# Optimization experiments

Hardware: AMD Instinct MI355X
Metric: run time of the kernel (lower is better)

The kernel has to match this reference:

```python
import jax, jax.numpy as jnp
import numpy as np

B, L, C, R, DK = 8, 2048, 512, 64, 64
H = 2 * C  # hdnSize
NEG = -32767.0  # -2**15 + 1
EPS = 1e-5


def _p(key, shape, std=0.02):
    return (jax.random.normal(key, shape, dtype=jnp.float32) * std)


def setup_inputs() -> dict:
    key = jax.random.key(0)
    ks = jax.random.split(key, 16)
    inp = {
        "x": jax.random.normal(ks[0], (B, L, C), dtype=jnp.float32),
        "maskPAD": jax.random.randint(ks[1], (B, 1, L), 0, 2, dtype=jnp.int32),
        "preScores": jax.random.normal(ks[2], (B, R, R), dtype=jnp.float32),
        "Wp": _p(ks[3], (C, R)), "bp": jnp.zeros((R,), jnp.float32),
        "Wq": _p(ks[4], (C, DK)), "bq": jnp.zeros((DK,), jnp.float32),
        "Wk": _p(ks[5], (C, DK)), "bk": jnp.zeros((DK,), jnp.float32),
        "Wv": _p(ks[6], (C, H)), "bv": jnp.zeros((H,), jnp.float32),
        "Wu": _p(ks[7], (C, H)), "bu": jnp.zeros((H,), jnp.float32),
        "Wo": _p(ks[8], (H, C)), "bo": jnp.zeros((C,), jnp.float32),
        "gamma": jnp.ones((C,), jnp.float32),
        "beta": jnp.zeros((C,), jnp.float32),
    }
    return inp


def reference(x, maskPAD, preScores, Wp, bp, Wq, bq, Wk, bk, Wv, bv, Wu, bu, Wo, bo, gamma, beta):
    # GLU gate: [B,L,H]
    gate = jax.nn.silu(x @ Wu + bu)
    # pseudo-attention logits [B,L,r], masked on padded positions
    pScore = x @ Wp + bp
    pad = (maskPAD[:, 0] == 0)[..., None]  # [B,L,1]
    pScore = jnp.where(pad, NEG, pScore)
    pAlpha = jax.nn.softmax(pScore, axis=1)    # softmax over L (dim=-2)
    pAlpha_ = jax.nn.softmax(pScore, axis=-1)  # softmax over r
    # compress: px [B,r,C]  (== pAlpha.transpose(-1,-2) @ x)
    px = jnp.einsum('blr,blc->brc', pAlpha, x)
    q = jax.nn.silu(px @ Wq + bq)  # [B,r,dk]
    k = jax.nn.silu(px @ Wk + bk)  # [B,r,dk]
    v = jax.nn.silu(px @ Wv + bv)  # [B,r,H]
    scores = jnp.einsum('brd,bsd->brs', q, k) / np.sqrt(DK).astype(np.float32)
    scores = scores + preScores
    alpha = jax.nn.softmax(scores, axis=2)
    z = alpha @ v                                # [B,r,H]
    z = jnp.einsum('blr,brh->blh', pAlpha_, z)   # expand back to [B,L,H]
    z = gate * z
    z = z @ Wo + bo                              # [B,L,C]
    y = x + z
    mu = jnp.mean(y, axis=-1, keepdims=True)
    var = jnp.var(y, axis=-1, keepdims=True)
    out = (y - mu) * jax.lax.rsqrt(var + EPS) * gamma + beta
    return out
```

## Files before the change

kernel.cpp:

```cpp
#include <hip/hip_runtime.h>
#include <hip/hip_bf16.h>

constexpr int B_ = 8;
constexpr int L_ = 2048;
constexpr int C_ = 512;
constexpr int R_ = 64;
constexpr int DK_ = 64;
constexpr int H_ = 1024;
constexpr int M_ = B_ * L_;
constexpr int NQKV_ = 1152;
constexpr float NEG_ = -32767.0f;

__device__ __forceinline__ float toF(float x) { return x; }
__device__ __forceinline__ float toF(__hip_bfloat16 x) { return __bfloat162float(x); }
__device__ __forceinline__ float siluf(float v) { return v / (1.0f + __expf(-v)); }
__device__ __forceinline__ ushort bfbits(float f) {
    __hip_bfloat16 h = __float2bfloat16(f);
    union { __hip_bfloat16 h; ushort u; } cv; cv.h = h; return cv.u;
}
__device__ __forceinline__ float bf2f(ushort u) {
    union { uint u; float f; } cv; cv.u = (uint)u << 16; return cv.f;
}

typedef __attribute__((ext_vector_type(8))) short bf16x8;
typedef __attribute__((ext_vector_type(4))) float f32x4;

#define GLOBAL_AS __attribute__((address_space(1)))
#define LDS_AS    __attribute__((address_space(3)))
__device__ __forceinline__ void glds16(const ushort* g, ushort* l) {
    __builtin_amdgcn_global_load_lds((const GLOBAL_AS void*)g, (LDS_AS void*)l, 16, 0, 0);
}

template <int EPI>
__global__ __launch_bounds__(256) void mfma_gemm5(
    const ushort* __restrict__ A, const ushort* __restrict__ Bt,
    const float* __restrict__ bias,
    const float* __restrict__ residF, const ushort* __restrict__ residB,
    const int* __restrict__ mask,
    ushort* __restrict__ outB, float* __restrict__ outF, float* __restrict__ outF2,
    int Ndim, int Kdim, int gridN, long bBatch)
{
    __shared__ ushort As[2][128 * 32];
    __shared__ ushort Bs[2][128 * 32];

    const int i = blockIdx.x;
    const int G = gridDim.x >> 3;
    const int gi = (gridDim.x & 7) ? i : ((i & 7) * G + (i >> 3));
    const int nt = gi % gridN, mt = gi / gridN;
    const int m0 = mt * 128, n0 = nt * 128;

    const int tid = threadIdx.x;
    const int lane = tid & 63, w = tid >> 6;
    const int wm = (w & 1) * 64, wn = (w >> 1) * 64;
    const int lr = lane & 15, lq = lane >> 4;

    const int sr = lane >> 2;
    const int sc = (lane & 3) * 8;
    const int s0 = w * 2, s1 = w * 2 + 1;

    const ushort* Bp = Bt + (bBatch ? (long)(m0 / L_) * bBatch : 0);
    int br0 = n0 + s0 * 16 + sr; if (br0 >= Ndim) br0 = Ndim - 1;
    int br1 = n0 + s1 * 16 + sr; if (br1 >= Ndim) br1 = Ndim - 1;
    const ushort* a0p = A  + (size_t)(m0 + s0 * 16 + sr) * Kdim + sc;
    const ushort* a1p = A  + (size_t)(m0 + s1 * 16 + sr) * Kdim + sc;
    const ushort* b0p = Bp + (size_t)br0 * Kdim + sc;
    const ushort* b1p = Bp + (size_t)br1 * Kdim + sc;
    const int lo0 = s0 * 512 + lane * 8;
    const int lo1 = s1 * 512 + lane * 8;

    f32x4 acc[4][4];
#pragma unroll
    for (int a = 0; a < 4; ++a)
#pragma unroll
        for (int b = 0; b < 4; ++b) acc[a][b] = (f32x4){0.f, 0.f, 0.f, 0.f};

    glds16(a0p, &As[0][lo0]);
    glds16(a1p, &As[0][lo1]);
    glds16(b0p, &Bs[0][lo0]);
    glds16(b1p, &Bs[0][lo1]);

    int cur = 0;
    for (int k0 = 0; k0 < Kdim; k0 += 32) {
        __syncthreads();
        if (k0 + 32 < Kdim) {
            const int nx = cur ^ 1;
            glds16(a0p + k0 + 32, &As[nx][lo0]);
            glds16(a1p + k0 + 32, &As[nx][lo1]);
            glds16(b0p + k0 + 32, &Bs[nx][lo0]);
            glds16(b1p + k0 + 32, &Bs[nx][lo1]);
        }
        bf16x8 af[4], bf[4];
#pragma unroll
        for (int a = 0; a < 4; ++a)
            af[a] = *(const bf16x8*)&As[cur][(wm + a * 16 + lr) * 32 + lq * 8];
#pragma unroll
        for (int b = 0; b < 4; ++b)
            bf[b] = *(const bf16x8*)&Bs[cur][(wn + b * 16 + lr) * 32 + lq * 8];
#pragma unroll
        for (int a = 0; a < 4; ++a)
#pragma unroll
            for (int b = 0; b < 4; ++b)
                acc[a][b] = __builtin_amdgcn_mfma_f32_16x16x32_bf16(af[a], bf[b], acc[a][b], 0, 0, 0);
        cur ^= 1;
    }

#pragma unroll
    for (int a = 0; a < 4; ++a) {
#pragma unroll
        for (int b = 0; b < 4; ++b) {
            const int col = n0 + wn + b * 16 + lr;
            if (col < Ndim) {
                const float bn = (EPI == 3) ? 0.f : bias[col];
#pragma unroll
                for (int r = 0; r < 4; ++r) {
                    const int row = m0 + wm + a * 16 + lq * 4 + r;
                    float v = acc[a][b][r];
                    if (EPI == 0) {
                        v = siluf(v + bn);
                        outB[(size_t)row * Ndim + col] = bfbits(v);
                    } else if (EPI == 2) {
                        v += bn + residF[(size_t)row * Ndim + col];
                        outB[(size_t)row * Ndim + col] = bfbits(v);
                    } else {
                        v *= bf2f(residB[(size_t)row * Ndim + col]);
                        outB[(size_t)row * Ndim + col] = bfbits(v);
                    }
                }
            }
        }
    }
}

__global__ __launch_bounds__(256) void pscore_gemm(
    const ushort* __restrict__ x16, const ushort* __restrict__ Wpt,
    const float* __restrict__ bp, const int* __restrict__ mask,
    ushort* __restrict__ pAR16, float* __restrict__ pScoreT)
{
    __shared__ ushort As[2][128 * 32];
    __shared__ ushort Bs[2][64 * 32];

    const int i = blockIdx.x;
    const int G = gridDim.x >> 3;
    const int gi = (i & 7) * G + (i >> 3);
    const int m0 = gi * 128;

    const int tid = threadIdx.x;
    const int lane = tid & 63, w = tid >> 6;
    const int lr = lane & 15, lq = lane >> 4;
    const int sr = lane >> 2, sc = (lane & 3) * 8;
    const int s0 = w * 2, s1 = w * 2 + 1;

    const ushort* a0p = x16 + (size_t)(m0 + s0 * 16 + sr) * C_ + sc;
    const ushort* a1p = x16 + (size_t)(m0 + s1 * 16 + sr) * C_ + sc;
    const ushort* bwp = Wpt + (size_t)(w * 16 + sr) * C_ + sc;
    const int lo0 = s0 * 512 + lane * 8;
    const int lo1 = s1 * 512 + lane * 8;
    const int lob = w * 512 + lane * 8;

    f32x4 acc[2][4];
#pragma unroll
    for (int a = 0; a < 2; ++a)
#pragma unroll
        for (int b = 0; b < 4; ++b) acc[a][b] = (f32x4){0.f, 0.f, 0.f, 0.f};

    glds16(a0p, &As[0][lo0]);
    glds16(a1p, &As[0][lo1]);
    glds16(bwp, &Bs[0][lob]);

    int cur = 0;
    for (int k0 = 0; k0 < C_; k0 += 32) {
        __syncthreads();
        if (k0 + 32 < C_) {
            const int nx = cur ^ 1;
            glds16(a0p + k0 + 32, &As[nx][lo0]);
            glds16(a1p + k0 + 32, &As[nx][lo1]);
            glds16(bwp + k0 + 32, &Bs[nx][lob]);
        }
        bf16x8 af[2], bf[4];
#pragma unroll
        for (int a = 0; a < 2; ++a)
            af[a] = *(const bf16x8*)&As[cur][(w * 32 + a * 16 + lr) * 32 + lq * 8];
#pragma unroll
        for (int b = 0; b < 4; ++b)
            bf[b] = *(const bf16x8*)&Bs[cur][(b * 16 + lr) * 32 + lq * 8];
#pragma unroll
        for (int a = 0; a < 2; ++a)
#pragma unroll
            for (int b = 0; b < 4; ++b)
                acc[a][b] = __builtin_amdgcn_mfma_f32_16x16x32_bf16(af[a], bf[b], acc[a][b], 0, 0, 0);
        cur ^= 1;
    }

#pragma unroll
    for (int a = 0; a < 2; ++a) {
#pragma unroll
        for (int r = 0; r < 4; ++r) {
            const int row = m0 + w * 32 + a * 16 + lq * 4 + r;
            const bool dead = (mask[row] == 0);
            const int bb = row >> 11, ll = row & (L_ - 1);
            float v[4];
            float mx = -3.4e38f;
#pragma unroll
            for (int b = 0; b < 4; ++b) {
                const int col = b * 16 + lr;
                float t = acc[a][b][r] + bp[col];
                if (dead) t = NEG_;
                v[b] = t;
                pScoreT[((size_t)bb * R_ + col) * L_ + ll] = t;
                mx = fmaxf(mx, t);
            }
#pragma unroll
            for (int o = 1; o < 16; o <<= 1) mx = fmaxf(mx, __shfl_xor(mx, o, 64));
            float e[4], s = 0.f;
#pragma unroll
            for (int b = 0; b < 4; ++b) { e[b] = __expf(v[b] - mx); s += e[b]; }
#pragma unroll
            for (int o = 1; o < 16; o <<= 1) s += __shfl_xor(s, o, 64);
            const float inv = 1.0f / s;
#pragma unroll
            for (int b = 0; b < 4; ++b)
                pAR16[(size_t)row * R_ + b * 16 + lr] = bfbits(e[b] * inv);
        }
    }
}

__global__ __launch_bounds__(256) void fused_gate_z(
    const ushort* __restrict__ x16, const ushort* __restrict__ Wut,
    const float* __restrict__ bu,
    const ushort* __restrict__ pAR, const ushort* __restrict__ zsT,
    ushort* __restrict__ zg)
{
    __shared__ ushort As[2][128 * 32];
    __shared__ ushort Bs[2][128 * 32];

    const int i = blockIdx.x;
    const int G = gridDim.x >> 3;
    const int gi = (i & 7) * G + (i >> 3);
    constexpr int gridN = H_ / 128;
    const int nt = gi % gridN, mt = gi / gridN;
    const int m0 = mt * 128, n0 = nt * 128;

    const int tid = threadIdx.x;
    const int lane = tid & 63, w = tid >> 6;
    const int wm = (w & 1) * 64, wn = (w >> 1) * 64;
    const int lr = lane & 15, lq = lane >> 4;
    const int sr = lane >> 2, sc = (lane & 3) * 8;
    const int s0 = w * 2, s1 = w * 2 + 1;

    const int bidx = m0 >> 11;
    const ushort* a0p = x16 + (size_t)(m0 + s0 * 16 + sr) * C_ + sc;
    const ushort* a1p = x16 + (size_t)(m0 + s1 * 16 + sr) * C_ + sc;
    const ushort* b0p = Wut + (size_t)(n0 + s0 * 16 + sr) * C_ + sc;
    const ushort* b1p = Wut + (size_t)(n0 + s1 * 16 + sr) * C_ + sc;
    const ushort* zb  = zsT + (size_t)bidx * H_ * R_;
    const ushort* c0p = pAR + (size_t)(m0 + s0 * 16 + sr) * R_ + sc;
    const ushort* c1p = pAR + (size_t)(m0 + s1 * 16 + sr) * R_ + sc;
    const ushort* d0p = zb + (size_t)(n0 + s0 * 16 + sr) * R_ + sc;
    const ushort* d1p = zb + (size_t)(n0 + s1 * 16 + sr) * R_ + sc;
    const int lo0 = s0 * 512 + lane * 8;
    const int lo1 = s1 * 512 + lane * 8;

    f32x4 acc[4][4];
#pragma unroll
    for (int a = 0; a < 4; ++a)
#pragma unroll
        for (int b = 0; b < 4; ++b) acc[a][b] = (f32x4){0.f, 0.f, 0.f, 0.f};

    glds16(c0p, &As[0][lo0]);
    glds16(c1p, &As[0][lo1]);
    glds16(d0p, &Bs[0][lo0]);
    glds16(d1p, &Bs[0][lo1]);

    int cur = 0;
#pragma unroll
    for (int kt = 0; kt < 2; ++kt) {
        __syncthreads();
        if (kt == 0) {
            glds16(c0p + 32, &As[1][lo0]);
            glds16(c1p + 32, &As[1][lo1]);
            glds16(d0p + 32, &Bs[1][lo0]);
            glds16(d1p + 32, &Bs[1][lo1]);
        } else {
            glds16(a0p, &As[0][lo0]);
            glds16(a1p, &As[0][lo1]);
            glds16(b0p, &Bs[0][lo0]);
            glds16(b1p, &Bs[0][lo1]);
        }
        bf16x8 af[4], bf[4];
#pragma unroll
        for (int a = 0; a < 4; ++a)
            af[a] = *(const bf16x8*)&As[cur][(wm + a * 16 + lr) * 32 + lq * 8];
#pragma unroll
        for (int b = 0; b < 4; ++b)
            bf[b] = *(const bf16x8*)&Bs[cur][(wn + b * 16 + lr) * 32 + lq * 8];
#pragma unroll
        for (int a = 0; a < 4; ++a)
#pragma unroll
            for (int b = 0; b < 4; ++b)
                acc[a][b] = __builtin_amdgcn_mfma_f32_16x16x32_bf16(af[a], bf[b], acc[a][b], 0, 0, 0);
        cur ^= 1;
    }

    uint pk[4][4][2];
#pragma unroll
    for (int a = 0; a < 4; ++a)
#pragma unroll
        for (int b = 0; b < 4; ++b) {
            pk[a][b][0] = (uint)bfbits(acc[a][b][0]) | ((uint)bfbits(acc[a][b][1]) << 16);
            pk[a][b][1] = (uint)bfbits(acc[a][b][2]) | ((uint)bfbits(acc[a][b][3]) << 16);
            acc[a][b] = (f32x4){0.f, 0.f, 0.f, 0.f};
        }

    for (int k0 = 0; k0 < C_; k0 += 32) {
        __syncthreads();
        if (k0 + 32 < C_) {
            const int nx = cur ^ 1;
            glds16(a0p + k0 + 32, &As[nx][lo0]);
            glds16(a1p + k0 + 32, &As[nx][lo1]);
            glds16(b0p + k0 + 32, &Bs[nx][lo0]);
            glds16(b1p + k0 + 32, &Bs[nx][lo1]);
        }
        bf16x8 af[4], bf[4];
#pragma unroll
        for (int a = 0; a < 4; ++a)
            af[a] = *(const bf16x8*)&As[cur][(wm + a * 16 + lr) * 32 + lq * 8];
#pragma unroll
        for (int b = 0; b < 4; ++b)
            bf[b] = *(const bf16x8*)&Bs[cur][(wn + b * 16 + lr) * 32 + lq * 8];
#pragma unroll
        for (int a = 0; a < 4; ++a)
#pragma unroll
            for (int b = 0; b < 4; ++b)
                acc[a][b] = __builtin_amdgcn_mfma_f32_16x16x32_bf16(af[a], bf[b], acc[a][b], 0, 0, 0);
        cur ^= 1;
    }

#pragma unroll
    for (int a = 0; a < 4; ++a) {
#pragma unroll
        for (int b = 0; b < 4; ++b) {
            const int col = n0 + wn + b * 16 + lr;
            const float bn = bu[col];
#pragma unroll
            for (int r = 0; r < 4; ++r) {
                const int row = m0 + wm + a * 16 + lq * 4 + r;
                const ushort zu = (ushort)((r & 1) ? (pk[a][b][r >> 1] >> 16)
                                                   : (pk[a][b][r >> 1] & 0xffff));
                const float v = siluf(acc[a][b][r] + bn) * bf2f(zu);
                zg[(size_t)row * H_ + col] = bfbits(v);
            }
        }
    }
}

__global__ __launch_bounds__(256) void x_prep(const float* __restrict__ x,
                                              ushort* __restrict__ x16,
                                              ushort* __restrict__ xT16)
{
    __shared__ float tile[32][33];
    const int tx = threadIdx.x & 31, ty = threadIdx.x >> 5;
    const int c0 = blockIdx.x * 32, l0 = blockIdx.y * 32;
#pragma unroll
    for (int i = 0; i < 32; i += 8) {
        const float v = x[(size_t)(l0 + ty + i) * C_ + c0 + tx];
        tile[ty + i][tx] = v;
        x16[(size_t)(l0 + ty + i) * C_ + c0 + tx] = bfbits(v);
    }
    __syncthreads();
    const int bb = l0 >> 11, ll0 = l0 & (L_ - 1);
#pragma unroll
    for (int i = 0; i < 32; i += 8)
        xT16[((size_t)bb * C_ + c0 + ty + i) * L_ + ll0 + tx] = bfbits(tile[tx][ty + i]);
}

__global__ __launch_bounds__(256) void prep_w(
    const float* __restrict__ Wu, const float* __restrict__ Wo, const float* __restrict__ Wp,
    const float* __restrict__ Wq, const float* __restrict__ bq,
    const float* __restrict__ Wk, const float* __restrict__ bk,
    const float* __restrict__ Wv, const float* __restrict__ bv,
    ushort* __restrict__ Wut, ushort* __restrict__ Wot, ushort* __restrict__ Wpt,
    ushort* __restrict__ Wqkvt, float* __restrict__ bqkv)
{
    int id = blockIdx.x;
    const float* W; ushort* Wt; const float* bsrc = nullptr;
    int K, Nloc, n0, k0, nn0;
    if (id < 512) {
        W = Wu; Wt = Wut; K = 512; Nloc = 1024;
        n0 = (id & 31) * 32; k0 = (id >> 5) * 32; nn0 = n0;
    } else if (id < 1024) {
        id -= 512; W = Wo; Wt = Wot; K = 1024; Nloc = 512;
        n0 = (id & 15) * 32; k0 = (id >> 4) * 32; nn0 = n0;
    } else if (id < 1056) {
        id -= 1024; W = Wp; Wt = Wpt; K = 512; Nloc = 64;
        n0 = (id & 1) * 32; k0 = (id >> 1) * 32; nn0 = n0;
    } else {
        id -= 1056; K = 512; Wt = Wqkvt;
        n0 = (id % 36) * 32; k0 = (id / 36) * 32;
        if (n0 < 64)       { W = Wq; bsrc = bq; Nloc = 64;   nn0 = n0; }
        else if (n0 < 128) { W = Wk; bsrc = bk; Nloc = 64;   nn0 = n0 - 64; }
        else               { W = Wv; bsrc = bv; Nloc = 1024; nn0 = n0 - 128; }
    }
    __shared__ float tile[32][33];
    const int tx = threadIdx.x & 31, ty = threadIdx.x >> 5;
#pragma unroll
    for (int i = 0; i < 32; i += 8)
        tile[ty + i][tx] = W[(size_t)(k0 + ty + i) * Nloc + nn0 + tx];
    __syncthreads();
#pragma unroll
    for (int i = 0; i < 32; i += 8)
        Wt[(size_t)(n0 + ty + i) * K + k0 + tx] = bfbits(tile[tx][ty + i]);
    if (bsrc && k0 == 0 && threadIdx.x < 32) bqkv[n0 + threadIdx.x] = bsrc[nn0 + threadIdx.x];
}

__global__ __launch_bounds__(256) void softmaxL2(const float* __restrict__ pScoreT,
                                                 ushort* __restrict__ pALT)
{
    const size_t br = blockIdx.x;
    const float* row = pScoreT + br * L_;
    ushort* orow = pALT + br * L_;
    const int t = threadIdx.x;
    __shared__ float red[256];

    float v[8];
    float mx = -3.4e38f;
#pragma unroll
    for (int j = 0; j < 8; ++j) { v[j] = row[t + j * 256]; mx = fmaxf(mx, v[j]); }
    red[t] = mx; __syncthreads();
    for (int s = 128; s > 0; s >>= 1) { if (t < s) red[t] = fmaxf(red[t], red[t + s]); __syncthreads(); }
    mx = red[0]; __syncthreads();

    float e[8], sum = 0.f;
#pragma unroll
    for (int j = 0; j < 8; ++j) { e[j] = __expf(v[j] - mx); sum += e[j]; }
    red[t] = sum; __syncthreads();
    for (int s = 128; s > 0; s >>= 1) { if (t < s) red[t] += red[t + s]; __syncthreads(); }
    const float inv = 1.0f / red[0];
#pragma unroll
    for (int j = 0; j < 8; ++j) orow[t + j * 256] = bfbits(e[j] * inv);
}

__global__ __launch_bounds__(512) void compress_mfma(
    const ushort* __restrict__ pALT, const ushort* __restrict__ xT,
    float* __restrict__ parts)
{
    __shared__ ushort As[2][64 * 32];
    __shared__ ushort Bs[2][256 * 32];

    const int bidx = blockIdx.y;
    const int n0 = blockIdx.x * 256;
    const int ks = blockIdx.z;
    const int kbeg = ks * (L_ / 4), kend = kbeg + L_ / 4;
    const int tid = threadIdx.x;
    const int lane = tid & 63, w = tid >> 6;
    const int lr = lane & 15, lq = lane >> 4;
    const int sr = lane >> 2, sc = (lane & 3) * 8;
    const int wm = (w & 1) * 32, wn = (w >> 1) * 64;

    const ushort* Ab = pALT + (size_t)bidx * R_ * L_;
    const ushort* Bb = xT + (size_t)bidx * C_ * L_;

    const int aseg = (w >= 4) ? (w - 4) : 0;
    const ushort* ap = Ab + (size_t)(aseg * 16 + sr) * L_ + sc;
    const int alo = aseg * 512 + lane * 8;
    const ushort* b0p = Bb + (size_t)(n0 + (w * 2) * 16 + sr) * L_ + sc;
    const ushort* b1p = Bb + (size_t)(n0 + (w * 2 + 1) * 16 + sr) * L_ + sc;
    const int blo0 = (w * 2) * 512 + lane * 8;
    const int blo1 = (w * 2 + 1) * 512 + lane * 8;

    f32x4 acc[2][4];
#pragma unroll
    for (int a = 0; a < 2; ++a)
#pragma unroll
        for (int b = 0; b < 4; ++b) acc[a][b] = (f32x4){0.f, 0.f, 0.f, 0.f};

    if (w >= 4) glds16(ap + kbeg, &As[0][alo]);
    glds16(b0p + kbeg, &Bs[0][blo0]);
    glds16(b1p + kbeg, &Bs[0][blo1]);

    int cur = 0;
    for (int k0 = kbeg; k0 < kend; k0 += 32) {
        __syncthreads();
        if (k0 + 32 < kend) {
            const int nx = cur ^ 1;
            if (w >= 4) glds16(ap + k0 + 32, &As[nx][alo]);
            glds16(b0p + k0 + 32, &Bs[nx][blo0]);
            glds16(b1p + k0 + 32, &Bs[nx][blo1]);
        }
        bf16x8 af[2], bf[4];
#pragma unroll
        for (int a = 0; a < 2; ++a)
            af[a] = *(const bf16x8*)&As[cur][(wm + a * 16 + lr) * 32 + lq * 8];
#pragma unroll
        for (int b = 0; b < 4; ++b)
            bf[b] = *(const bf16x8*)&Bs[cur][(wn + b * 16 + lr) * 32 + lq * 8];
#pragma unroll
        for (int a = 0; a < 2; ++a)
#pragma unroll
            for (int b = 0; b < 4; ++b)
                acc[a][b] = __builtin_amdgcn_mfma_f32_16x16x32_bf16(af[a], bf[b], acc[a][b], 0, 0, 0);
        cur ^= 1;
    }
#pragma unroll
    for (int a = 0; a < 2; ++a)
#pragma unroll
        for (int b = 0; b < 4; ++b)
#pragma unroll
            for (int r = 0; r < 4; ++r) {
                const int row = wm + a * 16 + lq * 4 + r;
                const int col = n0 + wn + b * 16 + lr;
                parts[(((size_t)ks * B_ + bidx) * R_ + row) * C_ + col] = acc[a][b][r];
            }
}

__global__ __launch_bounds__(256) void compress_reduce16(const float* __restrict__ parts,
                                                         ushort* __restrict__ px16)
{
    const size_t i = ((size_t)blockIdx.x * 256 + threadIdx.x) * 4;
    constexpr size_t S = (size_t)B_ * R_ * C_;
    const float4 a = *(const float4*)(parts + i);
    const float4 b = *(const float4*)(parts + i + S);
    const float4 c = *(const float4*)(parts + i + 2 * S);
    const float4 d = *(const float4*)(parts + i + 3 * S);
    ushort4 o;
    o.x = bfbits(a.x + b.x + c.x + d.x);
    o.y = bfbits(a.y + b.y + c.y + d.y);
    o.z = bfbits(a.z + b.z + c.z + d.z);
    o.w = bfbits(a.w + b.w + c.w + d.w);
    *(ushort4*)(px16 + i) = o;
}

__global__ __launch_bounds__(256) void attn_fused(
    const ushort* __restrict__ qkv, const float* __restrict__ preS,
    ushort* __restrict__ zsT)
{
    const int b = blockIdx.x >> 6, r = blockIdx.x & 63;
    const int t = threadIdx.x;
    __shared__ float al[R_];
    if (t < 64) {
        const ushort* qr = qkv + (size_t)(b * R_ + r) * NQKV_;
        const ushort* ks = qkv + (size_t)(b * R_ + t) * NQKV_ + 64;
        float acc = 0.f;
#pragma unroll
        for (int d = 0; d < DK_; d += 4) {
            const ushort4 qa = *(const ushort4*)(qr + d);
            const ushort4 ka = *(const ushort4*)(ks + d);
            acc += bf2f(qa.x) * bf2f(ka.x) + bf2f(qa.y) * bf2f(ka.y)
                 + bf2f(qa.z) * bf2f(ka.z) + bf2f(qa.w) * bf2f(ka.w);
        }
        acc = acc * 0.125f + preS[((size_t)b * R_ + r) * R_ + t];
        float mx = acc;
#pragma unroll
        for (int o = 32; o > 0; o >>= 1) mx = fmaxf(mx, __shfl_xor(mx, o, 64));
        float e = __expf(acc - mx);
        float sm = e;
#pragma unroll
        for (int o = 32; o > 0; o >>= 1) sm += __shfl_xor(sm, o, 64);
        al[t] = e / sm;
    }
    __syncthreads();
    float acc[4] = {};
    for (int s = 0; s < R_; ++s) {
        const float a = al[s];
        const ushort* vr = qkv + (size_t)(b * R_ + s) * NQKV_ + 128;
#pragma unroll
        for (int j = 0; j < 4; ++j) acc[j] += a * bf2f(vr[t + j * 256]);
    }
#pragma unroll
    for (int j = 0; j < 4; ++j) {
        const int h = t + j * 256;
        zsT[((size_t)b * H_ + h) * R_ + r] = bfbits(acc[j]);
    }
}

__global__ __launch_bounds__(256) void layernorm(const __hip_bfloat16* __restrict__ y,
                                                 const float* __restrict__ gamma,
                                                 const float* __restrict__ beta,
                                                 float* __restrict__ out)
{
    const size_t m = blockIdx.x;
    const int t = threadIdx.x;
    const __hip_bfloat16* yr = y + m * C_;
    float v0 = __bfloat162float(yr[t]), v1 = __bfloat162float(yr[t + 256]);
    __shared__ float rs[256], rq[256];
    rs[t] = v0 + v1;
    rq[t] = v0 * v0 + v1 * v1;
    __syncthreads();
    for (int o = 128; o > 0; o >>= 1) {
        if (t < o) { rs[t] += rs[t + o]; rq[t] += rq[t + o]; }
        __syncthreads();
    }
    const float mu = rs[0] * (1.0f / C_);
    const float var = rq[0] * (1.0f / C_) - mu * mu;
    const float inv = rsqrtf(var + 1e-5f);
    out[m * C_ + t] = (v0 - mu) * inv * gamma[t] + beta[t];
    out[m * C_ + t + 256] = (v1 - mu) * inv * gamma[t + 256] + beta[t + 256];
}

template <typename AT, typename BT, typename RT, int ACT, int EPI>
__global__ __launch_bounds__(256) void gemm64(
    const AT* __restrict__ A, const BT* __restrict__ Bw,
    const float* __restrict__ bias, const int* __restrict__ mask,
    const RT* resid, float* __restrict__ outF, __hip_bfloat16* outB,
    int Ndim, int Kdim, long bBatchStride)
{
    __shared__ float As[16][68];
    __shared__ float Bs[16][64];
    const int tid = threadIdx.x;
    const int tx = tid & 15, ty = tid >> 4;
    const int n0 = blockIdx.x * 64, m0 = blockIdx.y * 64;
    const BT* Bp = Bw + (bBatchStride ? (long)(m0 / L_) * bBatchStride : 0);
    float acc[4][4] = {};
    for (int k0 = 0; k0 < Kdim; k0 += 16) {
#pragma unroll
        for (int s = 0; s < 4; ++s) {
            int idx = tid + s * 256;
            int am = idx >> 4, ak = idx & 15;
            As[ak][am] = toF(A[(size_t)(m0 + am) * Kdim + k0 + ak]);
        }
#pragma unroll
        for (int s = 0; s < 4; ++s) {
            int idx = tid + s * 256;
            int bk = idx >> 6, bn = idx & 63;
            Bs[bk][bn] = toF(Bp[(size_t)(k0 + bk) * Ndim + n0 + bn]);
        }
        __syncthreads();
#pragma unroll
        for (int kk = 0; kk < 16; ++kk) {
            float av[4], bv[4];
            *(float4*)av = *(const float4*)&As[kk][ty * 4];
            *(float4*)bv = *(const float4*)&Bs[kk][tx * 4];
#pragma unroll
            for (int i = 0; i < 4; ++i)
#pragma unroll
                for (int j = 0; j < 4; ++j) acc[i][j] += av[i] * bv[j];
        }
        __syncthreads();
    }
#pragma unroll
    for (int i = 0; i < 4; ++i) {
        int m = m0 + ty * 4 + i;
#pragma unroll
        for (int j = 0; j < 4; ++j) {
            int n = n0 + tx * 4 + j;
            float val = acc[i][j];
            if (EPI != 3) val += bias[n];
            if (ACT) val = siluf(val);
            if (EPI == 0) outB[(size_t)m * Ndim + n] = __float2bfloat16(val);
            else if (EPI == 1) { if (mask[m] == 0) val = NEG_; outF[(size_t)m * Ndim + n] = val; }
            else if (EPI == 2) { val += toF(resid[(size_t)m * Ndim + n]); outB[(size_t)m * Ndim + n] = __float2bfloat16(val); }
            else { val *= toF(resid[(size_t)m * Ndim + n]); outB[(size_t)m * Ndim + n] = __float2bfloat16(val); }
        }
    }
}

template <int OUT>
__global__ __launch_bounds__(64) void softmaxR(const float* __restrict__ pScore,
                                               float* __restrict__ outF,
                                               ushort* __restrict__ outU)
{
    const size_t m = blockIdx.x;
    const int t = threadIdx.x;
    float v = pScore[m * R_ + t];
    float mx = v;
#pragma unroll
    for (int o = 32; o > 0; o >>= 1) mx = fmaxf(mx, __shfl_xor(mx, o, 64));
    float e = __expf(v - mx);
    float s = e;
#pragma unroll
    for (int o = 32; o > 0; o >>= 1) s += __shfl_xor(s, o, 64);
    if (OUT == 0) outF[m * R_ + t] = e / s;
    else          outU[m * R_ + t] = bfbits(e / s);
}

__global__ __launch_bounds__(256) void softmaxL(const float* __restrict__ pScore,
                                                float* __restrict__ pAlpha)
{
    const int b = blockIdx.x >> 6, r = blockIdx.x & 63;
    const int t = threadIdx.x;
    const float* base = pScore + (size_t)b * L_ * R_ + r;
    float* out = pAlpha + (size_t)b * L_ * R_ + r;
    __shared__ float red[256];
    float mx = -3.4e38f;
    for (int l = t; l < L_; l += 256) mx = fmaxf(mx, base[(size_t)l * R_]);
    red[t] = mx; __syncthreads();
    for (int s = 128; s > 0; s >>= 1) { if (t < s) red[t] = fmaxf(red[t], red[t + s]); __syncthreads(); }
    mx = red[0]; __syncthreads();
    float sum = 0.f;
    for (int l = t; l < L_; l += 256) {
        float e = __expf(base[(size_t)l * R_] - mx);
        out[(size_t)l * R_] = e; sum += e;
    }
    red[t] = sum; __syncthreads();
    for (int s = 128; s > 0; s >>= 1) { if (t < s) red[t] += red[t + s]; __syncthreads(); }
    const float inv = 1.0f / red[0];
    for (int l = t; l < L_; l += 256) out[(size_t)l * R_] *= inv;
}

__global__ __launch_bounds__(256) void compress_part(
    const float* __restrict__ pAlpha, const float* __restrict__ x,
    float* __restrict__ parts)
{
    __shared__ float As[16][64];
    __shared__ float Bs[16][64];
    const int tid = threadIdx.x;
    const int tx = tid & 15, ty = tid >> 4;
    const int n0 = blockIdx.x * 64;
    const int ks = blockIdx.y;
    const int b  = blockIdx.z;
    const float* pa = pAlpha + (size_t)b * L_ * R_;
    const float* xb = x + (size_t)b * L_ * C_;
    float acc[4][4] = {};
    const int kbeg = ks * (L_ / 4), kend = kbeg + L_ / 4;
    for (int k0 = kbeg; k0 < kend; k0 += 16) {
#pragma unroll
        for (int s = 0; s < 4; ++s) {
            int idx = tid + s * 256;
            int kk = idx >> 6, m = idx & 63;
            As[kk][m] = pa[(size_t)(k0 + kk) * R_ + m];
        }
#pragma unroll
        for (int s = 0; s < 4; ++s) {
            int idx = tid + s * 256;
            int kk = idx >> 6, n = idx & 63;
            Bs[kk][n] = xb[(size_t)(k0 + kk) * C_ + n0 + n];
        }
        __syncthreads();
#pragma unroll
        for (int kk = 0; kk < 16; ++kk) {
            float av[4], bv[4];
            *(float4*)av = *(const float4*)&As[kk][ty * 4];
            *(float4*)bv = *(const float4*)&Bs[kk][tx * 4];
#pragma unroll
            for (int i = 0; i < 4; ++i)
#pragma unroll
                for (int j = 0; j < 4; ++j) acc[i][j] += av[i] * bv[j];
        }
        __syncthreads();
    }
#pragma unroll
    for (int i = 0; i < 4; ++i)
#pragma unroll
        for (int j = 0; j < 4; ++j)
            parts[((((size_t)ks * B_ + b) * R_) + ty * 4 + i) * C_ + n0 + tx * 4 + j] = acc[i][j];
}

__global__ __launch_bounds__(256) void compress_reduce(const float* __restrict__ parts,
                                                       float* __restrict__ px)
{
    const size_t i = (size_t)blockIdx.x * 256 + threadIdx.x;
    constexpr size_t S = (size_t)B_ * R_ * C_;
    px[i] = parts[i] + parts[i + S] + parts[i + 2 * S] + parts[i + 3 * S];
}

__global__ __launch_bounds__(256) void qkv_gemm(
    const float* __restrict__ px,
    const float* __restrict__ Wq, const float* __restrict__ bq,
    const float* __restrict__ Wk, const float* __restrict__ bk,
    const float* __restrict__ Wv, const float* __restrict__ bv,
    float* __restrict__ q, float* __restrict__ k, float* __restrict__ v)
{
    __shared__ float As[16][68];
    __shared__ float Bs[16][64];
    const int tid = threadIdx.x;
    const int tx = tid & 15, ty = tid >> 4;
    const int bx = blockIdx.x;
    const int m0 = blockIdx.y * 64;
    const float* W; const float* bias; float* dst; int Nloc, ncol0;
    if (bx == 0)      { W = Wq; bias = bq; dst = q; Nloc = 64;   ncol0 = 0; }
    else if (bx == 1) { W = Wk; bias = bk; dst = k; Nloc = 64;   ncol0 = 0; }
    else              { W = Wv; bias = bv; dst = v; Nloc = H_;   ncol0 = (bx - 2) * 64; }

    float acc[4][4] = {};
    for (int k0 = 0; k0 < C_; k0 += 16) {
#pragma unroll
        for (int s = 0; s < 4; ++s) {
            int idx = tid + s * 256;
            int am = idx >> 4, ak = idx & 15;
            As[ak][am] = px[(size_t)(m0 + am) * C_ + k0 + ak];
        }
#pragma unroll
        for (int s = 0; s < 4; ++s) {
            int idx = tid + s * 256;
            int kk = idx >> 6, bn = idx & 63;
            Bs[kk][bn] = W[(size_t)(k0 + kk) * Nloc + ncol0 + bn];
        }
        __syncthreads();
#pragma unroll
        for (int kk = 0; kk < 16; ++kk) {
            float av[4], bv4[4];
            *(float4*)av = *(const float4*)&As[kk][ty * 4];
            *(float4*)bv4 = *(const float4*)&Bs[kk][tx * 4];
#pragma unroll
            for (int i = 0; i < 4; ++i)
#pragma unroll
                for (int j = 0; j < 4; ++j) acc[i][j] += av[i] * bv4[j];
        }
        __syncthreads();
    }
#pragma unroll
    for (int i = 0; i < 4; ++i) {
        int m = m0 + ty * 4 + i;
#pragma unroll
        for (int j = 0; j < 4; ++j) {
            int n = ncol0 + tx * 4 + j;
            dst[(size_t)m * Nloc + n] = siluf(acc[i][j] + bias[n]);
        }
    }
}

template <int MODE>
__global__ __launch_bounds__(256) void attn_z(const float* __restrict__ alpha,
                                              const float* __restrict__ v,
                                              float* __restrict__ zsF,
                                              ushort* __restrict__ zsT)
{
    const int b = blockIdx.x >> 6, r = blockIdx.x & 63;
    const int t = threadIdx.x;
    __shared__ float al[R_];
    if (t < R_) al[t] = alpha[((size_t)b * R_ + r) * R_ + t];
    __syncthreads();
    float acc[4] = {};
    for (int s = 0; s < R_; ++s) {
        float a = al[s];
        const float* vr = v + ((size_t)b * R_ + s) * H_;
#pragma unroll
        for (int j = 0; j < 4; ++j) acc[j] += a * vr[t + j * 256];
    }
#pragma unroll
    for (int j = 0; j < 4; ++j) {
        const int h = t + j * 256;
        if (MODE == 0) zsF[((size_t)b * R_ + r) * H_ + h] = acc[j];
        else           zsT[((size_t)b * H_ + h) * R_ + r] = bfbits(acc[j]);
    }
}

__global__ __launch_bounds__(64) void attn_scores(
    const float* __restrict__ q, const float* __restrict__ k,
    const float* __restrict__ preS, float* __restrict__ alpha)
{
    const int b = blockIdx.x >> 6, r = blockIdx.x & 63;
    const int s = threadIdx.x;
    const float* qr = q + ((size_t)b * R_ + r) * DK_;
    const float* ks = k + ((size_t)b * R_ + s) * DK_;
    float acc = 0.f;
#pragma unroll
    for (int d = 0; d < DK_; ++d) acc += qr[d] * ks[d];
    acc = acc * 0.125f + preS[((size_t)b * R_ + r) * R_ + s];
    float mx = acc;
#pragma unroll
    for (int o = 32; o > 0; o >>= 1) mx = fmaxf(mx, __shfl_xor(mx, o, 64));
    float e = __expf(acc - mx);
    float sm = e;
#pragma unroll
    for (int o = 32; o > 0; o >>= 1) sm += __shfl_xor(sm, o, 64);
    alpha[((size_t)b * R_ + r) * R_ + s] = e / sm;
}

extern "C" void kernel_launch(void* const* d_in, const int* in_sizes, int n_in,
                              void* d_out, int out_size, void* d_ws, size_t ws_size,
                              hipStream_t stream)
{
    using bf16 = __hip_bfloat16;
    const float* x      = (const float*)d_in[0];
    const int*  maskPAD = (const int*)d_in[1];
    const float* preS   = (const float*)d_in[2];
    const float* Wp     = (const float*)d_in[3];
    const float* bp     = (const float*)d_in[4];
    const float* Wq     = (const float*)d_in[5];
    const float* bq     = (const float*)d_in[6];
    const float* Wk     = (const float*)d_in[7];
    const float* bk     = (const float*)d_in[8];
    const float* Wv     = (const float*)d_in[9];
    const float* bv     = (const float*)d_in[10];
    const float* Wu     = (const float*)d_in[11];
    const float* bu     = (const float*)d_in[12];
    const float* Wo     = (const float*)d_in[13];
    const float* bo     = (const float*)d_in[14];
    const float* gamma  = (const float*)d_in[15];
    const float* beta   = (const float*)d_in[16];
    float* out          = (float*)d_out;

    char* ws = (char*)d_ws;
    const bool bigWS = ws_size >= (size_t)52 * 1024 * 1024;

    if (bigWS) {
        bf16* zg = (bf16*)ws;
        float* parts = (float*)ws;
        char* pool = ws + (size_t)M_ * H_ * 2;
        float* pScoreT = (float*)pool;
        ushort* pALT   = (ushort*)(pScoreT + (size_t)B_ * R_ * L_);
        ushort* pAR16  = pALT + (size_t)B_ * R_ * L_;
        ushort* px16   = pAR16 + (size_t)M_ * R_;
        ushort* qkv16  = px16 + (size_t)B_ * R_ * C_;
        ushort* zsT16  = qkv16 + (size_t)B_ * R_ * NQKV_;
        ushort* Wqkvt  = zsT16 + (size_t)B_ * H_ * R_;
        float*  bqkv   = (float*)(Wqkvt + (size_t)NQKV_ * C_);
        bf16*  y       = (bf16*)pool;
        ushort* Wut    = (ushort*)(pool + 18221568);
        ushort* Wot    = Wut + (size_t)C_ * H_;
        ushort* Wpt    = Wot + (size_t)C_ * H_;
        ushort* x16    = (ushort*)d_out;
        ushort* xT16   = x16 + (size_t)M_ * C_;

        x_prep<<<dim3(C_ / 32, M_ / 32), 256, 0, stream>>>(x, x16, xT16);
        prep_w<<<1632, 256, 0, stream>>>(Wu, Wo, Wp, Wq, bq, Wk, bk, Wv, bv,
                                         Wut, Wot, Wpt, Wqkvt, bqkv);
        pscore_gemm<<<M_ / 128, 256, 0, stream>>>(x16, Wpt, bp, maskPAD, pAR16, pScoreT);
        softmaxL2<<<B_ * R_, 256, 0, stream>>>(pScoreT, pALT);
        compress_mfma<<<dim3(C_ / 256, B_, 4), 512, 0, stream>>>(pALT, xT16, parts);
        compress_reduce16<<<(B_ * R_ * C_) / 1024, 256, 0, stream>>>(parts, px16);
        mfma_gemm5<0><<<(NQKV_ / 128) * ((B_ * R_) / 128), 256, 0, stream>>>(
            px16, Wqkvt, bqkv, nullptr, nullptr, nullptr, qkv16, nullptr, nullptr,
            NQKV_, C_, NQKV_ / 128, 0);
        attn_fused<<<B_ * R_, 256, 0, stream>>>(qkv16, preS, zsT16);
        fused_gate_z<<<(H_ / 128) * (M_ / 128), 256, 0, stream>>>(
            x16, Wut, bu, pAR16, zsT16, (ushort*)zg);
        mfma_gemm5<2><<<(C_ / 128) * (M_ / 128), 256, 0, stream>>>(
            (ushort*)zg, Wot, bo, x, nullptr, nullptr, (ushort*)y, nullptr, nullptr,
            C_, H_, C_ / 128, 0);
        layernorm<<<M_, 256, 0, stream>>>(y, gamma, beta, out);
    } else {
        float* pScore = (float*)ws;
        float* pAL   = pScore + (size_t)M_ * R_;
        float* pAR   = pAL    + (size_t)M_ * R_;
        float* px    = pAR    + (size_t)M_ * R_;
        float* q     = px     + (size_t)B_ * R_ * C_;
        float* kk    = q      + (size_t)B_ * R_ * DK_;
        float* vv    = kk     + (size_t)B_ * R_ * DK_;
        float* alpha = vv     + (size_t)B_ * R_ * H_;
        float* zs    = alpha  + (size_t)B_ * R_ * R_;
        bf16* gate_b = (bf16*)(zs + (size_t)B_ * R_ * H_);
        bf16* y_b    = (bf16*)((char*)gate_b + (size_t)L_ * H_ * 2);

        gemm64<float, float, float, 0, 1><<<dim3(R_ / 64, M_ / 64), 256, 0, stream>>>(
            x, Wp, bp, maskPAD, (const float*)nullptr, pScore, nullptr, R_, C_, 0);
        softmaxL<<<B_ * R_, 256, 0, stream>>>(pScore, pAL);
        softmaxR<0><<<M_, 64, 0, stream>>>(pScore, pAR, nullptr);
        compress_part<<<dim3(C_ / 64, 4, B_), 256, 0, stream>>>(pAL, x, pScore);
        compress_reduce<<<(B_ * R_ * C_) / 256, 256, 0, stream>>>(pScore, px);
        qkv_gemm<<<dim3(2 + H_ / 64, (B_ * R_) / 64), 256, 0, stream>>>(
            px, Wq, bq, Wk, bk, Wv, bv, q, kk, vv);
        attn_scores<<<B_ * R_, 64, 0, stream>>>(q, kk, preS, alpha);
        attn_z<0><<<B_ * R_, 256, 0, stream>>>(alpha, vv, zs, nullptr);

        for (int b = 0; b < B_; ++b) {
            const float* xb = x + (size_t)b * L_ * C_;
            gemm64<float, float, float, 1, 0><<<dim3(H_ / 64, L_ / 64), 256, 0, stream>>>(
                xb, Wu, bu, nullptr, (const float*)nullptr, nullptr, gate_b, H_, C_, 0);
            gemm64<float, float, bf16, 0, 3><<<dim3(H_ / 64, L_ / 64), 256, 0, stream>>>(
                pAR + (size_t)b * L_ * R_, zs + (size_t)b * R_ * H_,
                nullptr, nullptr, gate_b, nullptr, gate_b, H_, R_, 0);
            gemm64<bf16, float, float, 0, 2><<<dim3(C_ / 64, L_ / 64), 256, 0, stream>>>(
                gate_b, Wo, bo, nullptr, xb, nullptr, y_b, C_, H_, 0);
            layernorm<<<L_, 256, 0, stream>>>(y_b, gamma, beta, out + (size_t)b * L_ * C_);
        }
    }
}
```

Measured before the change: 267.2 us.

## Triple-buffer LDS staging with explicit vmcnt waits in all MFMA GEMMs

Converts the double-buffered global_load_lds pipelines in four GEMM kernels to triple buffering with a prefetch distance of two K-steps. A partial s_waitcnt vmcnt plus a raw s_barrier replaces __syncthreads, so loads for later tiles can stay in flight across the barrier. The gated GEMM's two-phase loop is merged into one 18-step pipeline. The cost is 50% more LDS per block, which may lower occupancy, and correctness now depends on hand-counted vmcnt values.

```diff
diff --git a/kernel.cpp b/kernel.cpp
--- a/kernel.cpp
+++ b/kernel.cpp
@@ -31,6 +31,9 @@
     __builtin_amdgcn_global_load_lds((const GLOBAL_AS void*)g, (LDS_AS void*)l, 16, 0, 0);
 }
 
+#define VMCNT(n) asm volatile("s_waitcnt vmcnt(" #n ")" ::: "memory")
+#define BARRIER() do { __builtin_amdgcn_s_barrier(); asm volatile("" ::: "memory"); } while (0)
+
 template <int EPI>
 __global__ __launch_bounds__(256) void mfma_gemm5(
     const ushort* __restrict__ A, const ushort* __restrict__ Bt,
@@ -40,8 +43,8 @@
     ushort* __restrict__ outB, float* __restrict__ outF, float* __restrict__ outF2,
     int Ndim, int Kdim, int gridN, long bBatch)
 {
-    __shared__ ushort As[2][128 * 32];
-    __shared__ ushort Bs[2][128 * 32];
+    __shared__ ushort As[3][128 * 32];
+    __shared__ ushort Bs[3][128 * 32];
 
     const int i = blockIdx.x;
     const int G = gridDim.x >> 3;
@@ -78,16 +81,23 @@
     glds16(a1p, &As[0][lo1]);
     glds16(b0p, &Bs[0][lo0]);
     glds16(b1p, &Bs[0][lo1]);
+    if (32 < Kdim) {
+        glds16(a0p + 32, &As[1][lo0]);
+        glds16(a1p + 32, &As[1][lo1]);
+        glds16(b0p + 32, &Bs[1][lo0]);
+        glds16(b1p + 32, &Bs[1][lo1]);
+    }
 
     int cur = 0;
     for (int k0 = 0; k0 < Kdim; k0 += 32) {
-        __syncthreads();
-        if (k0 + 32 < Kdim) {
-            const int nx = cur ^ 1;
-            glds16(a0p + k0 + 32, &As[nx][lo0]);
-            glds16(a1p + k0 + 32, &As[nx][lo1]);
-            glds16(b0p + k0 + 32, &Bs[nx][lo0]);
-            glds16(b1p + k0 + 32, &Bs[nx][lo1]);
+        if (k0 + 32 < Kdim) VMCNT(4); else VMCNT(0);
+        BARRIER();
+        if (k0 + 64 < Kdim) {
+            const int nx = cur ? cur - 1 : 2;
+            glds16(a0p + k0 + 64, &As[nx][lo0]);
+            glds16(a1p + k0 + 64, &As[nx][lo1]);
+            glds16(b0p + k0 + 64, &Bs[nx][lo0]);
+            glds16(b1p + k0 + 64, &Bs[nx][lo1]);
         }
         bf16x8 af[4], bf[4];
 #pragma unroll
@@ -101,7 +111,7 @@
 #pragma unroll
             for (int b = 0; b < 4; ++b)
                 acc[a][b] = __builtin_amdgcn_mfma_f32_16x16x32_bf16(af[a], bf[b], acc[a][b], 0, 0, 0);
-        cur ^= 1;
+        cur = (cur == 2) ? 0 : cur + 1;
     }
 
 #pragma unroll
@@ -136,8 +146,8 @@
     const float* __restrict__ bp, const int* __restrict__ mask,
     ushort* __restrict__ pAR16, float* __restrict__ pScoreT)
 {
-    __shared__ ushort As[2][128 * 32];
-    __shared__ ushort Bs[2][64 * 32];
+    __shared__ ushort As[3][128 * 32];
+    __shared__ ushort Bs[3][64 * 32];
 
     const int i = blockIdx.x;
     const int G = gridDim.x >> 3;
@@ -166,15 +176,19 @@
     glds16(a0p, &As[0][lo0]);
     glds16(a1p, &As[0][lo1]);
     glds16(bwp, &Bs[0][lob]);
+    glds16(a0p + 32, &As[1][lo0]);
+    glds16(a1p + 32, &As[1][lo1]);
+    glds16(bwp + 32, &Bs[1][lob]);
 
     int cur = 0;
     for (int k0 = 0; k0 < C_; k0 += 32) {
-        __syncthreads();
-        if (k0 + 32 < C_) {
-            const int nx = cur ^ 1;
-            glds16(a0p + k0 + 32, &As[nx][lo0]);
-            glds16(a1p + k0 + 32, &As[nx][lo1]);
-            glds16(bwp + k0 + 32, &Bs[nx][lob]);
+        if (k0 + 32 < C_) VMCNT(3); else VMCNT(0);
+        BARRIER();
+        if (k0 + 64 < C_) {
+            const int nx = cur ? cur - 1 : 2;
+            glds16(a0p + k0 + 64, &As[nx][lo0]);
+            glds16(a1p + k0 + 64, &As[nx][lo1]);
+            glds16(bwp + k0 + 64, &Bs[nx][lob]);
         }
         bf16x8 af[2], bf[4];
 #pragma unroll
@@ -188,7 +202,7 @@
 #pragma unroll
             for (int b = 0; b < 4; ++b)
                 acc[a][b] = __builtin_amdgcn_mfma_f32_16x16x32_bf16(af[a], bf[b], acc[a][b], 0, 0, 0);
-        cur ^= 1;
+        cur = (cur == 2) ? 0 : cur + 1;
     }
 
 #pragma unroll
@@ -230,8 +244,8 @@
     const ushort* __restrict__ pAR, const ushort* __restrict__ zsT,
     ushort* __restrict__ zg)
 {
-    __shared__ ushort As[2][128 * 32];
-    __shared__ ushort Bs[2][128 * 32];
+    __shared__ ushort As[3][128 * 32];
+    __shared__ ushort Bs[3][128 * 32];
 
     const int i = blockIdx.x;
     const int G = gridDim.x >> 3;
@@ -260,32 +274,38 @@
     const int lo0 = s0 * 512 + lane * 8;
     const int lo1 = s1 * 512 + lane * 8;
 
+    auto stage = [&](int t, int bsel) {
+        if (t < 2) {
+            const int off = t * 32;
+            glds16(c0p + off, &As[bsel][lo0]);
+            glds16(c1p + off, &As[bsel][lo1]);
+            glds16(d0p + off, &Bs[bsel][lo0]);
+            glds16(d1p + off, &Bs[bsel][lo1]);
+        } else {
+            const int off = (t - 2) * 32;
+            glds16(a0p + off, &As[bsel][lo0]);
+            glds16(a1p + off, &As[bsel][lo1]);
+            glds16(b0p + off, &Bs[bsel][lo0]);
+            glds16(b1p + off, &Bs[bsel][lo1]);
+        }
+    };
+
     f32x4 acc[4][4];
 #pragma unroll
     for (int a = 0; a < 4; ++a)
 #pragma unroll
         for (int b = 0; b < 4; ++b) acc[a][b] = (f32x4){0.f, 0.f, 0.f, 0.f};
 
-    glds16(c0p, &As[0][lo0]);
-    glds16(c1p, &As[0][lo1]);
-    glds16(d0p, &Bs[0][lo0]);
-    glds16(d1p, &Bs[0][lo1]);
+    uint pk[4][4][2];
+
+    stage(0, 0);
+    stage(1, 1);
 
     int cur = 0;
-#pragma unroll
-    for (int kt = 0; kt < 2; ++kt) {
-        __syncthreads();
-        if (kt == 0) {
-            glds16(c0p + 32, &As[1][lo0]);
-            glds16(c1p + 32, &As[1][lo1]);
-            glds16(d0p + 32, &Bs[1][lo0]);
-            glds16(d1p + 32, &Bs[1][lo1]);
-        } else {
-            glds16(a0p, &As[0][lo0]);
-            glds16(a1p, &As[0][lo1]);
-            glds16(b0p, &Bs[0][lo0]);
-            glds16(b1p, &Bs[0][lo1]);
-        }
+    for (int t = 0; t < 18; ++t) {
+        if (t < 17) VMCNT(4); else VMCNT(0);
+        BARRIER();
+        if (t + 2 < 18) stage(t + 2, cur ? cur - 1 : 2);
         bf16x8 af[4], bf[4];
 #pragma unroll
         for (int a = 0; a < 4; ++a)
@@ -298,41 +318,17 @@
 #pragma unroll
             for (int b = 0; b < 4; ++b)
                 acc[a][b] = __builtin_amdgcn_mfma_f32_16x16x32_bf16(af[a], bf[b], acc[a][b], 0, 0, 0);
-        cur ^= 1;
-    }
-
-    uint pk[4][4][2];
-#pragma unroll
-    for (int a = 0; a < 4; ++a)
-#pragma unroll
-        for (int b = 0; b < 4; ++b) {
-            pk[a][b][0] = (uint)bfbits(acc[a][b][0]) | ((uint)bfbits(acc[a][b][1]) << 16);
-            pk[a][b][1] = (uint)bfbits(acc[a][b][2]) | ((uint)bfbits(acc[a][b][3]) << 16);
-            acc[a][b] = (f32x4){0.f, 0.f, 0.f, 0.f};
-        }
-
-    for (int k0 = 0; k0 < C_; k0 += 32) {
-        __syncthreads();
-        if (k0 + 32 < C_) {
-            const int nx = cur ^ 1;
-            glds16(a0p + k0 + 32, &As[nx][lo0]);
-            glds16(a1p + k0 + 32, &As[nx][lo1]);
-            glds16(b0p + k0 + 32, &Bs[nx][lo0]);
-            glds16(b1p + k0 + 32, &Bs[nx][lo1]);
-        }
-        bf16x8 af[4], bf[4];
-#pragma unroll
-        for (int a = 0; a < 4; ++a)
-            af[a] = *(const bf16x8*)&As[cur][(wm + a * 16 + lr) * 32 + lq * 8];
-#pragma unroll
-        for (int b = 0; b < 4; ++b)
-            bf[b] = *(const bf16x8*)&Bs[cur][(wn + b * 16 + lr) * 32 + lq * 8];
-#pragma unroll
-        for (int a = 0; a < 4; ++a)
-#pragma unroll
-            for (int b = 0; b < 4; ++b)
-                acc[a][b] = __builtin_amdgcn_mfma_f32_16x16x32_bf16(af[a], bf[b], acc[a][b], 0, 0, 0);
-        cur ^= 1;
+        if (t == 1) {
+#pragma unroll
+            for (int a = 0; a < 4; ++a)
+#pragma unroll
+                for (int b = 0; b < 4; ++b) {
+                    pk[a][b][0] = (uint)bfbits(acc[a][b][0]) | ((uint)bfbits(acc[a][b][1]) << 16);
+                    pk[a][b][1] = (uint)bfbits(acc[a][b][2]) | ((uint)bfbits(acc[a][b][3]) << 16);
+                    acc[a][b] = (f32x4){0.f, 0.f, 0.f, 0.f};
+                }
+        }
+        cur = (cur == 2) ? 0 : cur + 1;
     }
 
 #pragma unroll
@@ -443,8 +439,8 @@
     const ushort* __restrict__ pALT, const ushort* __restrict__ xT,
     float* __restrict__ parts)
 {
-    __shared__ ushort As[2][64 * 32];
-    __shared__ ushort Bs[2][256 * 32];
+    __shared__ ushort As[3][64 * 32];
+    __shared__ ushort Bs[3][256 * 32];
 
     const int bidx = blockIdx.y;
     const int n0 = blockIdx.x * 256;
@@ -467,25 +463,30 @@
     const int blo0 = (w * 2) * 512 + lane * 8;
     const int blo1 = (w * 2 + 1) * 512 + lane * 8;
 
+    auto stage = [&](int k0, int bsel) {
+        if (w >= 4) glds16(ap + k0, &As[bsel][alo]);
+        glds16(b0p + k0, &Bs[bsel][blo0]);
+        glds16(b1p + k0, &Bs[bsel][blo1]);
+    };
+
     f32x4 acc[2][4];
 #pragma unroll
     for (int a = 0; a < 2; ++a)
 #pragma unroll
         for (int b = 0; b < 4; ++b) acc[a][b] = (f32x4){0.f, 0.f, 0.f, 0.f};
 
-    if (w >= 4) glds16(ap + kbeg, &As[0][alo]);
-    glds16(b0p + kbeg, &Bs[0][blo0]);
-    glds16(b1p + kbeg, &Bs[0][blo1]);
+    stage(kbeg, 0);
+    stage(kbeg + 32, 1);
 
     int cur = 0;
     for (int k0 = kbeg; k0 < kend; k0 += 32) {
-        __syncthreads();
         if (k0 + 32 < kend) {
-            const int nx = cur ^ 1;
-            if (w >= 4) glds16(ap + k0 + 32, &As[nx][alo]);
-            glds16(b0p + k0 + 32, &Bs[nx][blo0]);
-            glds16(b1p + k0 + 32, &Bs[nx][blo1]);
-        }
+            if (w >= 4) VMCNT(3); else VMCNT(2);
+        } else {
+            VMCNT(0);
+        }
+        BARRIER();
+        if (k0 + 64 < kend) stage(k0 + 64, cur ? cur - 1 : 2);
         bf16x8 af[2], bf[4];
 #pragma unroll
         for (int a = 0; a < 2; ++a)
@@ -498,7 +499,7 @@
 #pragma unroll
             for (int b = 0; b < 4; ++b)
                 acc[a][b] = __builtin_amdgcn_mfma_f32_16x16x32_bf16(af[a], bf[b], acc[a][b], 0, 0, 0);
-        cur ^= 1;
+        cur = (cur == 2) ? 0 : cur + 1;
     }
 #pragma unroll
     for (int a = 0; a < 2; ++a)
```

Measured after the change: 268.3 us. No clear change (+0.4%).
